# Performance work log

Hardware: AMD Instinct MI355X
Metric: run time of the kernel (lower is better)

## Reference

```python
import jax, jax.numpy as jnp
import numpy as np

B, C, H, W = 2048, 4, 84, 84
FEAT = 7 * 7 * 64  # 3136, from 84->20->9->7 conv arithmetic
D = 512
E = 6            # num_experts
K = 2            # top_k
A = 12           # output_dim (actions)


def _conv(x, w, b, stride):
    y = jax.lax.conv_general_dilated(
        x, w, window_strides=(stride, stride), padding='VALID',
        dimension_numbers=('NCHW', 'OIHW', 'NCHW'))
    return y + b[None, :, None, None]


def setup_inputs() -> dict:
    key = jax.random.key(0)
    ks = jax.random.split(key, 16)
    s = lambda k, shape, fan: jax.random.normal(k, shape, jnp.float32) * (1.0 / np.sqrt(fan))
    return {
        'x': jax.random.normal(ks[0], (B, C, H, W), jnp.float32),
        'c1_w': s(ks[1], (32, C, 8, 8), C * 64), 'c1_b': jnp.zeros((32,), jnp.float32),
        'c2_w': s(ks[2], (64, 32, 4, 4), 32 * 16), 'c2_b': jnp.zeros((64,), jnp.float32),
        'c3_w': s(ks[3], (64, 64, 3, 3), 64 * 9), 'c3_b': jnp.zeros((64,), jnp.float32),
        'fc_w': s(ks[4], (FEAT, D), FEAT), 'fc_b': jnp.zeros((D,), jnp.float32),
        'gate_w': s(ks[5], (D, E), D), 'gate_b': jnp.zeros((E,), jnp.float32),
        'e_w1': s(ks[6], (E, D, D), D), 'e_b1': jnp.zeros((E, D), jnp.float32),
        'e_w2': s(ks[7], (E, D, D), D), 'e_b2': jnp.zeros((E, D), jnp.float32),
        'e_w3': s(ks[8], (E, D, A), D), 'e_b3': jnp.zeros((E, A), jnp.float32),
    }


def reference(x, c1_w, c1_b, c2_w, c2_b, c3_w, c3_b, fc_w, fc_b,
              gate_w, gate_b, e_w1, e_b1, e_w2, e_b2, e_w3, e_b3):
    # CNN feature extractor (dropout omitted: eval semantics)
    h = jax.nn.relu(_conv(x, c1_w, c1_b, 4))
    h = jax.nn.relu(_conv(h, c2_w, c2_b, 2))
    h = jax.nn.relu(_conv(h, c3_w, c3_b, 1))
    h = h.reshape(h.shape[0], -1)                     # [B, 3136] (C,H,W flatten order)
    f = jax.nn.relu(h @ fc_w + fc_b)                  # [B, 512]

    # Gating: softmax -> top-2 -> renormalize
    gate_probs = jax.nn.softmax(f @ gate_w + gate_b, axis=-1)    # [B, E]
    top_p, top_i = jax.lax.top_k(gate_probs, K)                   # [B, K]
    top_p = top_p / jnp.sum(top_p, axis=-1, keepdims=True)

    # Experts: compute all (tiny MLPs), then gather top-k outputs
    h1 = jax.nn.relu(jnp.einsum('bd,edh->beh', f, e_w1) + e_b1)   # [B, E, D]
    h2 = jax.nn.relu(jnp.einsum('beh,ehg->beg', h1, e_w2) + e_b2) # [B, E, D]
    eo = jnp.einsum('beg,ego->beo', h2, e_w3) + e_b3              # [B, E, A]
    sel = jnp.take_along_axis(eo, top_i[:, :, None], axis=1)      # [B, K, A]
    out = jnp.sum(sel * top_p[:, :, None], axis=1)                # [B, A]
    return out
```

## Files before the change

kernel.cpp:

```cpp
#include <hip/hip_runtime.h>
#include <hip/hip_bf16.h>
#include <math.h>

typedef __attribute__((ext_vector_type(8))) short bf16x8;
typedef __attribute__((ext_vector_type(4))) float f32x4;

__device__ __forceinline__ float b2f(unsigned short u) {
    unsigned int v = ((unsigned int)u) << 16;
    return __uint_as_float(v);
}
__device__ __forceinline__ unsigned short f2b(float f) {
    __hip_bfloat16 h = __float2bfloat16(f);
    return *reinterpret_cast<unsigned short*>(&h);
}
__device__ __forceinline__ void split_trunc(float v, short& h, short& l) {
    unsigned int ui = __float_as_uint(v);
    h = (short)(ui >> 16);
    float hf = __uint_as_float(ui & 0xffff0000u);
    l = (short)f2b(v - hf);
}

__global__ __launch_bounds__(256) void prep_w(
    const float* __restrict__ w1, const float* __restrict__ w2, const float* __restrict__ w3,
    const float* __restrict__ ew3,
    unsigned short* __restrict__ wb1h, unsigned short* __restrict__ wb1l,
    unsigned short* __restrict__ w2h, unsigned short* __restrict__ w2l,
    unsigned short* __restrict__ w3h, unsigned short* __restrict__ w3l,
    float* __restrict__ w3t) {
    int tid = blockIdx.x * 256 + threadIdx.x;
    if (tid < 8192) {
        int k = tid >> 8, r = tid & 255;
        int c = r >> 6, ky = (r >> 3) & 7, kx = r & 7;
        float v = w1[tid];
        unsigned short h = f2b(v);
        int d = ((ky * 2 + (k >> 4)) * 16 + (k & 15)) * 32 + c * 8 + kx;
        wb1h[d] = h;
        wb1l[d] = f2b(v - b2f(h));
    } else if (tid < 8192 + 32768) {
        int i = tid - 8192;
        int n = i >> 9, r = i & 511;
        int c = r >> 4, ky = (r >> 2) & 3, kx = r & 3;
        float v = w2[i];
        unsigned short h = f2b(v);
        int d = ((ky * 4 + kx) * 64 + n) * 32 + c;
        w2h[d] = h;
        w2l[d] = f2b(v - b2f(h));
    } else if (tid < 8192 + 32768 + 36864) {
        int i = tid - 40960;
        int n = i / 576, r = i - n * 576;
        int c = r / 9, s = r - c * 9;
        int ky = s / 3, kx = s - ky * 3;
        float v = w3[i];
        unsigned short h = f2b(v);
        int d = (((ky * 3 + kx) * 2 + (c >> 5)) * 64 + n) * 32 + (c & 31);
        w3h[d] = h;
        w3l[d] = f2b(v - b2f(h));
    } else if (tid < 77824 + 36864) {
        int i = tid - 77824;
        int e = i / 6144, rem = i - e * 6144;
        int a = rem >> 9, k = rem & 511;
        w3t[i] = ew3[e * 6144 + k * 12 + a];
    }
}

__global__ __launch_bounds__(256) void prep_fcw(
    const float* __restrict__ fw, unsigned short* __restrict__ h, unsigned short* __restrict__ l) {
    __shared__ float tile[64][65];
    int k0 = blockIdx.x * 64;
    int n0 = blockIdx.y * 64;
    int tx = threadIdx.x & 63, ty = threadIdx.x >> 6;
#pragma unroll
    for (int j = 0; j < 16; j++) {
        int kk = ty + j * 4;
        int kp = k0 + kk;
        int p = kp >> 6, c = kp & 63;
        tile[kk][tx] = fw[(c * 49 + p) * 512 + n0 + tx];
    }
    __syncthreads();
#pragma unroll
    for (int j = 0; j < 16; j++) {
        int r = ty + j * 4;
        float v = tile[tx][r];
        unsigned short hh = f2b(v);
        long d = (long)(n0 + r) * 3136 + k0 + tx;
        h[d] = hh;
        l[d] = f2b(v - b2f(hh));
    }
}

__global__ __launch_bounds__(256) void prep_ewT(
    const float* __restrict__ ew1, const float* __restrict__ ew2,
    unsigned short* __restrict__ t1, unsigned short* __restrict__ t2) {
    __shared__ float tile[32][33];
    int z = blockIdx.z;
    int e = z % 6;
    const float* src = (z < 6) ? (ew1 + e * 262144) : (ew2 + e * 262144);
    unsigned short* dst = (z < 6) ? (t1 + e * 262144) : (t2 + e * 262144);
    int d0 = blockIdx.y * 32;
    int h0 = blockIdx.x * 32;
    int tx = threadIdx.x, ty = threadIdx.y;
#pragma unroll
    for (int j = 0; j < 4; j++)
        tile[ty + j * 8][tx] = src[(d0 + ty + j * 8) * 512 + h0 + tx];
    __syncthreads();
#pragma unroll
    for (int j = 0; j < 4; j++)
        dst[(h0 + ty + j * 8) * 512 + (d0 + tx)] = f2b(tile[tx][ty + j * 8]);
}

__global__ __launch_bounds__(256, 3) void conv1_k(
    const float* __restrict__ x, const unsigned short* __restrict__ wbh,
    const unsigned short* __restrict__ wbl, const float* __restrict__ b1,
    unsigned short* __restrict__ yhi, unsigned short* __restrict__ ylo) {
    int t = threadIdx.x;
    int wave = t >> 6, lane = t & 63, l16 = lane & 15, quad = lane >> 4;
    int px0 = blockIdx.x * 256 + wave * 64;
    const float* abase[4];
#pragma unroll
    for (int i = 0; i < 4; i++) {
        int px = px0 + i * 16 + l16;
        int n = px / 400;
        int rem = px - n * 400;
        int oy = rem / 20;
        int ox = rem - oy * 20;
        abase[i] = x + (long)n * 28224 + quad * 7056 + oy * 4 * 84 + ox * 4;
    }
    f32x4 acc[4][2];
#pragma unroll
    for (int i = 0; i < 4; i++)
#pragma unroll
        for (int j = 0; j < 2; j++)
#pragma unroll
            for (int r = 0; r < 4; r++) acc[i][j][r] = 0.f;
    float4 cur[8];
#pragma unroll
    for (int i = 0; i < 4; i++) {
        cur[i * 2] = *(const float4*)abase[i];
        cur[i * 2 + 1] = *(const float4*)(abase[i] + 4);
    }
#pragma unroll
    for (int ky = 0; ky < 8; ky++) {
        float4 nxt[8];
        if (ky < 7) {
#pragma unroll
            for (int i = 0; i < 4; i++) {
                const float* p = abase[i] + (ky + 1) * 84;
                nxt[i * 2] = *(const float4*)p;
                nxt[i * 2 + 1] = *(const float4*)(p + 4);
            }
        }
        int wo = (ky * 32 + l16) * 32 + quad * 8;
        bf16x8 bh0 = *(const bf16x8*)(wbh + wo);
        bf16x8 bh1 = *(const bf16x8*)(wbh + wo + 512);
        bf16x8 bl0 = *(const bf16x8*)(wbl + wo);
        bf16x8 bl1 = *(const bf16x8*)(wbl + wo + 512);
        bf16x8 ah[4], al[4];
#pragma unroll
        for (int i = 0; i < 4; i++) {
            float v[8] = {cur[i * 2].x, cur[i * 2].y, cur[i * 2].z, cur[i * 2].w,
                          cur[i * 2 + 1].x, cur[i * 2 + 1].y, cur[i * 2 + 1].z, cur[i * 2 + 1].w};
#pragma unroll
            for (int j = 0; j < 8; j++) {
                short hh, ll;
                split_trunc(v[j], hh, ll);
                ah[i][j] = hh;
                al[i][j] = ll;
            }
        }
#pragma unroll
        for (int i = 0; i < 4; i++) {
            acc[i][0] = __builtin_amdgcn_mfma_f32_16x16x32_bf16(ah[i], bh0, acc[i][0], 0, 0, 0);
            acc[i][0] = __builtin_amdgcn_mfma_f32_16x16x32_bf16(al[i], bh0, acc[i][0], 0, 0, 0);
            acc[i][0] = __builtin_amdgcn_mfma_f32_16x16x32_bf16(ah[i], bl0, acc[i][0], 0, 0, 0);
            acc[i][1] = __builtin_amdgcn_mfma_f32_16x16x32_bf16(ah[i], bh1, acc[i][1], 0, 0, 0);
            acc[i][1] = __builtin_amdgcn_mfma_f32_16x16x32_bf16(al[i], bh1, acc[i][1], 0, 0, 0);
            acc[i][1] = __builtin_amdgcn_mfma_f32_16x16x32_bf16(ah[i], bl1, acc[i][1], 0, 0, 0);
        }
        if (ky < 7) {
#pragma unroll
            for (int q = 0; q < 8; q++) cur[q] = nxt[q];
        }
    }
    float bias0 = b1[l16], bias1 = b1[16 + l16];
#pragma unroll
    for (int i = 0; i < 4; i++) {
#pragma unroll
        for (int r = 0; r < 4; r++) {
            long px = px0 + i * 16 + quad * 4 + r;
            long o = px * 32;
            float v0 = fmaxf(acc[i][0][r] + bias0, 0.f);
            float v1 = fmaxf(acc[i][1][r] + bias1, 0.f);
            short h0, l0, h1, l1;
            split_trunc(v0, h0, l0);
            split_trunc(v1, h1, l1);
            yhi[o + l16] = (unsigned short)h0;
            ylo[o + l16] = (unsigned short)l0;
            yhi[o + 16 + l16] = (unsigned short)h1;
            ylo[o + 16 + l16] = (unsigned short)l1;
        }
    }
}

template <int C, int IH, int IW, int OH, int OW, int S, int KH, int KW>
__global__ __launch_bounds__(64, 3) void convm_k(
    const unsigned short* __restrict__ xhi, const unsigned short* __restrict__ xlo,
    const unsigned short* __restrict__ whi, const unsigned short* __restrict__ wlo,
    const float* __restrict__ bias,
    unsigned short* __restrict__ yhi, unsigned short* __restrict__ ylo) {
    constexpr int CH = C / 32;
    constexpr int NCHUNK = KH * KW * CH;
    int lane = threadIdx.x, l16 = lane & 15, quad = lane >> 4;
    int pxbase = blockIdx.x * 64;
    long xoff[4];
#pragma unroll
    for (int i = 0; i < 4; i++) {
        int px = pxbase + i * 16 + l16;
        int n = px / (OH * OW);
        int rem = px - n * (OH * OW);
        int oy = rem / OW;
        int ox = rem - oy * OW;
        xoff[i] = (((long)n * IH + oy * S) * IW + ox * S) * C + quad * 8;
    }
    f32x4 acc[4][4];
#pragma unroll
    for (int i = 0; i < 4; i++)
#pragma unroll
        for (int j = 0; j < 4; j++)
#pragma unroll
            for (int r = 0; r < 4; r++) acc[i][j][r] = 0.f;
#pragma unroll 2
    for (int ck = 0; ck < NCHUNK; ck++) {
        int kyx = ck / CH;
        int ch = ck - kyx * CH;
        int ky = kyx / KW, kx = kyx - ky * KW;
        long koff = ((long)(ky * IW + kx)) * C + ch * 32;
        bf16x8 ah[4], al[4], bh[4], bl[4];
#pragma unroll
        for (int i = 0; i < 4; i++) {
            ah[i] = *(const bf16x8*)(xhi + xoff[i] + koff);
            al[i] = *(const bf16x8*)(xlo + xoff[i] + koff);
        }
#pragma unroll
        for (int j = 0; j < 4; j++) {
            long b = ((long)ck * 64 + j * 16 + l16) * 32 + quad * 8;
            bh[j] = *(const bf16x8*)(whi + b);
            bl[j] = *(const bf16x8*)(wlo + b);
        }
#pragma unroll
        for (int i = 0; i < 4; i++)
#pragma unroll
            for (int j = 0; j < 4; j++) {
                acc[i][j] = __builtin_amdgcn_mfma_f32_16x16x32_bf16(ah[i], bh[j], acc[i][j], 0, 0, 0);
                acc[i][j] = __builtin_amdgcn_mfma_f32_16x16x32_bf16(ah[i], bl[j], acc[i][j], 0, 0, 0);
                acc[i][j] = __builtin_amdgcn_mfma_f32_16x16x32_bf16(al[i], bh[j], acc[i][j], 0, 0, 0);
            }
    }
#pragma unroll
    for (int i = 0; i < 4; i++)
#pragma unroll
        for (int j = 0; j < 4; j++) {
            int col = j * 16 + l16;
            float bv = bias[col];
#pragma unroll
            for (int r = 0; r < 4; r++) {
                int prow = pxbase + i * 16 + quad * 4 + r;
                float v = fmaxf(acc[i][j][r] + bv, 0.f);
                unsigned short h = f2b(v);
                yhi[(long)prow * 64 + col] = h;
                ylo[(long)prow * 64 + col] = f2b(v - b2f(h));
            }
        }
}

__global__ __launch_bounds__(64, 3) void fc_k(
    const unsigned short* __restrict__ Ahi, const unsigned short* __restrict__ Alo,
    const unsigned short* __restrict__ Bhi, const unsigned short* __restrict__ Blo,
    float* __restrict__ Cp) {
    int lane = threadIdx.x, l16 = lane & 15, quad = lane >> 4;
    int m0 = blockIdx.x * 64, n0 = blockIdx.y * 64;
    int z = blockIdx.z;
    int kBase = z * 448;
    f32x4 acc[4][4];
#pragma unroll
    for (int i = 0; i < 4; i++)
#pragma unroll
        for (int j = 0; j < 4; j++)
#pragma unroll
            for (int r = 0; r < 4; r++) acc[i][j][r] = 0.f;
#pragma unroll 2
    for (int k0 = kBase; k0 < kBase + 448; k0 += 32) {
        bf16x8 ah[4], al[4], bh[4], bl[4];
#pragma unroll
        for (int i = 0; i < 4; i++) {
            long a = (long)(m0 + i * 16 + l16) * 3136 + k0 + quad * 8;
            ah[i] = *(const bf16x8*)(Ahi + a);
            al[i] = *(const bf16x8*)(Alo + a);
        }
#pragma unroll
        for (int j = 0; j < 4; j++) {
            long b = (long)(n0 + j * 16 + l16) * 3136 + k0 + quad * 8;
            bh[j] = *(const bf16x8*)(Bhi + b);
            bl[j] = *(const bf16x8*)(Blo + b);
        }
#pragma unroll
        for (int i = 0; i < 4; i++)
#pragma unroll
            for (int j = 0; j < 4; j++) {
                acc[i][j] = __builtin_amdgcn_mfma_f32_16x16x32_bf16(ah[i], bh[j], acc[i][j], 0, 0, 0);
                acc[i][j] = __builtin_amdgcn_mfma_f32_16x16x32_bf16(ah[i], bl[j], acc[i][j], 0, 0, 0);
                acc[i][j] = __builtin_amdgcn_mfma_f32_16x16x32_bf16(al[i], bh[j], acc[i][j], 0, 0, 0);
            }
    }
    float* Cz = Cp + (long)z * 1048576;
#pragma unroll
    for (int i = 0; i < 4; i++)
#pragma unroll
        for (int j = 0; j < 4; j++) {
            int col = n0 + j * 16 + l16;
#pragma unroll
            for (int r = 0; r < 4; r++) {
                int row = m0 + i * 16 + quad * 4 + r;
                Cz[row * 512 + col] = acc[i][j][r];
            }
        }
}

__global__ __launch_bounds__(256) void fc_fin(
    const float* __restrict__ Cp, const float* __restrict__ bias,
    float* __restrict__ f, unsigned short* __restrict__ fb) {
    int tid = blockIdx.x * 256 + threadIdx.x;
    int col = tid & 511;
    float v = bias[col];
#pragma unroll
    for (int z = 0; z < 7; z++) v += Cp[tid + (long)z * 1048576];
    v = fmaxf(v, 0.f);
    f[tid] = v;
    fb[tid] = f2b(v);
}

__global__ __launch_bounds__(256) void gate_k(
    const float* __restrict__ f, const float* __restrict__ gw, const float* __restrict__ gb,
    int* __restrict__ topi, float* __restrict__ topp) {
    int wave = threadIdx.x >> 6, lane = threadIdx.x & 63;
    int row = blockIdx.x * 4 + wave;
    float fv[8];
#pragma unroll
    for (int j = 0; j < 8; j++) fv[j] = f[row * 512 + lane + 64 * j];
    float lg[6];
#pragma unroll
    for (int e = 0; e < 6; e++) {
        float a = 0.f;
#pragma unroll
        for (int j = 0; j < 8; j++) a += fv[j] * gw[(lane + 64 * j) * 6 + e];
#pragma unroll
        for (int off = 32; off > 0; off >>= 1) a += __shfl_xor(a, off, 64);
        lg[e] = a + gb[e];
    }
    if (lane == 0) {
        int i1 = 0;
        float v1 = lg[0];
#pragma unroll
        for (int e = 1; e < 6; e++)
            if (lg[e] > v1) { v1 = lg[e]; i1 = e; }
        int i2 = (i1 == 0) ? 1 : 0;
        float v2 = lg[i2];
#pragma unroll
        for (int e = 0; e < 6; e++)
            if (e != i1 && lg[e] > v2) { v2 = lg[e]; i2 = e; }
        float pa = 1.f / (1.f + expf(v2 - v1));
        topi[row * 2] = i1;
        topi[row * 2 + 1] = i2;
        topp[row * 2] = pa;
        topp[row * 2 + 1] = 1.f - pa;
    }
}

__global__ __launch_bounds__(64, 4) void moe_gemm(
    const unsigned short* __restrict__ A, long aStride,
    const unsigned short* __restrict__ Bt, const float* __restrict__ bias,
    unsigned short* __restrict__ C) {
    int e = blockIdx.z;
    const unsigned short* Ae = A + (long)e * aStride;
    const unsigned short* Be = Bt + (long)e * 262144;
    const float* be = bias + e * 512;
    unsigned short* Ce = C + (long)e * 2048 * 512;
    int lane = threadIdx.x, l16 = lane & 15, quad = lane >> 4;
    int m0 = blockIdx.x * 64, n0 = blockIdx.y * 64;
    f32x4 acc[4][4];
#pragma unroll
    for (int i = 0; i < 4; i++)
#pragma unroll
        for (int j = 0; j < 4; j++)
#pragma unroll
            for (int r = 0; r < 4; r++) acc[i][j][r] = 0.f;
#pragma unroll 4
    for (int k0 = 0; k0 < 512; k0 += 32) {
        bf16x8 a[4], b[4];
#pragma unroll
        for (int i = 0; i < 4; i++)
            a[i] = *(const bf16x8*)(Ae + (long)(m0 + i * 16 + l16) * 512 + k0 + quad * 8);
#pragma unroll
        for (int j = 0; j < 4; j++)
            b[j] = *(const bf16x8*)(Be + (long)(n0 + j * 16 + l16) * 512 + k0 + quad * 8);
#pragma unroll
        for (int i = 0; i < 4; i++)
#pragma unroll
            for (int j = 0; j < 4; j++)
                acc[i][j] = __builtin_amdgcn_mfma_f32_16x16x32_bf16(a[i], b[j], acc[i][j], 0, 0, 0);
    }
#pragma unroll
    for (int i = 0; i < 4; i++)
#pragma unroll
        for (int j = 0; j < 4; j++) {
            int col = n0 + j * 16 + l16;
            float bcol = be[col];
#pragma unroll
            for (int r = 0; r < 4; r++) {
                int row = m0 + i * 16 + quad * 4 + r;
                float v = fmaxf(acc[i][j][r] + bcol, 0.f);
                Ce[(long)row * 512 + col] = f2b(v);
            }
        }
}

__global__ __launch_bounds__(256) void combine_k(
    const unsigned short* __restrict__ h2, const float* __restrict__ w3t,
    const float* __restrict__ b3, const int* __restrict__ topi,
    const float* __restrict__ topp, float* __restrict__ out) {
    int b = blockIdx.x * 4 + (threadIdx.x >> 6);
    int lane = threadIdx.x & 63;
    int e0 = topi[b * 2], e1 = topi[b * 2 + 1];
    float p0 = topp[b * 2], p1 = topp[b * 2 + 1];
    float r[12];
#pragma unroll
    for (int a = 0; a < 12; a++) r[a] = 0.f;
#pragma unroll
    for (int j = 0; j < 2; j++) {
        int e = j ? e1 : e0;
        float p = j ? p1 : p0;
        const unsigned short* hp = h2 + ((long)e * 2048 + b) * 512 + lane * 8;
        bf16x8 hv = *(const bf16x8*)hp;
        float hf[8];
#pragma unroll
        for (int q = 0; q < 8; q++) hf[q] = b2f((unsigned short)hv[q]);
        const float* wb = w3t + e * 6144 + lane * 8;
#pragma unroll
        for (int a = 0; a < 12; a++) {
            float4 w0 = *(const float4*)(wb + a * 512);
            float4 w1 = *(const float4*)(wb + a * 512 + 4);
            float acc = hf[0] * w0.x + hf[1] * w0.y + hf[2] * w0.z + hf[3] * w0.w +
                        hf[4] * w1.x + hf[5] * w1.y + hf[6] * w1.z + hf[7] * w1.w;
            r[a] += p * acc;
        }
    }
#pragma unroll
    for (int a = 0; a < 12; a++)
#pragma unroll
        for (int off = 32; off > 0; off >>= 1) r[a] += __shfl_xor(r[a], off, 64);
    float v = 0.f;
#pragma unroll
    for (int a = 0; a < 12; a++)
        if (lane == a) v = r[a];
    if (lane < 12)
        out[b * 12 + lane] = v + p0 * b3[e0 * 12 + lane] + p1 * b3[e1 * 12 + lane];
}

extern "C" void kernel_launch(void* const* d_in, const int* in_sizes, int n_in,
                              void* d_out, int out_size, void* d_ws, size_t ws_size,
                              hipStream_t stream) {
    const float* x   = (const float*)d_in[0];
    const float* c1w = (const float*)d_in[1];
    const float* c1b = (const float*)d_in[2];
    const float* c2w = (const float*)d_in[3];
    const float* c2b = (const float*)d_in[4];
    const float* c3w = (const float*)d_in[5];
    const float* c3b = (const float*)d_in[6];
    const float* fcw = (const float*)d_in[7];
    const float* fcb = (const float*)d_in[8];
    const float* gw  = (const float*)d_in[9];
    const float* gb  = (const float*)d_in[10];
    const float* ew1 = (const float*)d_in[11];
    const float* eb1 = (const float*)d_in[12];
    const float* ew2 = (const float*)d_in[13];
    const float* eb2 = (const float*)d_in[14];
    const float* ew3 = (const float*)d_in[15];
    const float* eb3 = (const float*)d_in[16];

    char* ws = (char*)d_ws;
    unsigned short* y1hi = (unsigned short*)(ws + 0L);
    unsigned short* y1lo = (unsigned short*)(ws + 52428800L);
    unsigned short* f3hi = (unsigned short*)(ws + 0L);
    unsigned short* f3lo = (unsigned short*)(ws + 12845056L);
    unsigned short* y2hi = (unsigned short*)(ws + 104857600L);
    unsigned short* y2lo = (unsigned short*)(ws + 126091264L);
    unsigned short* h1   = (unsigned short*)(ws + 104857600L);
    unsigned short* h2   = (unsigned short*)(ws + 117440512L);
    float* f             = (float*)(ws + 147324928L);
    unsigned short* fb   = (unsigned short*)(ws + 151519232L);
    int*   topi          = (int*)(ws + 153616384L);
    float* topp          = (float*)(ws + 153632768L);
    unsigned short* w2h  = (unsigned short*)(ws + 153681920L);
    unsigned short* w2l  = (unsigned short*)(ws + 153747456L);
    unsigned short* w3h  = (unsigned short*)(ws + 153812992L);
    unsigned short* w3l  = (unsigned short*)(ws + 153886720L);
    unsigned short* fcwh = (unsigned short*)(ws + 153960448L);
    unsigned short* fcwl = (unsigned short*)(ws + 157171712L);
    unsigned short* ew1t = (unsigned short*)(ws + 160382976L);
    unsigned short* ew2t = (unsigned short*)(ws + 163528704L);
    float* w3t           = (float*)(ws + 166674432L);
    float* Cp            = (float*)(ws + 166821888L);
    unsigned short* wb1h = (unsigned short*)(ws + 196182016L);
    unsigned short* wb1l = (unsigned short*)(ws + 196198400L);
    float* out = (float*)d_out;

    hipLaunchKernelGGL(prep_w, dim3(448), dim3(256), 0, stream, c1w, c2w, c3w, ew3,
                       wb1h, wb1l, w2h, w2l, w3h, w3l, w3t);
    hipLaunchKernelGGL(prep_fcw, dim3(49, 8), dim3(256), 0, stream, fcw, fcwh, fcwl);
    hipLaunchKernelGGL(prep_ewT, dim3(16, 16, 12), dim3(32, 8), 0, stream, ew1, ew2, ew1t, ew2t);
    hipLaunchKernelGGL(conv1_k, dim3(3200), dim3(256), 0, stream, x, wb1h, wb1l, c1b, y1hi, y1lo);
    hipLaunchKernelGGL((convm_k<32, 20, 20, 9, 9, 2, 4, 4>), dim3(2592), dim3(64), 0, stream,
                       y1hi, y1lo, w2h, w2l, c2b, y2hi, y2lo);
    hipLaunchKernelGGL((convm_k<64, 9, 9, 7, 7, 1, 3, 3>), dim3(1568), dim3(64), 0, stream,
                       y2hi, y2lo, w3h, w3l, c3b, f3hi, f3lo);
    hipLaunchKernelGGL(fc_k, dim3(32, 8, 7), dim3(64), 0, stream, f3hi, f3lo, fcwh, fcwl, Cp);
    hipLaunchKernelGGL(fc_fin, dim3(4096), dim3(256), 0, stream, Cp, fcb, f, fb);
    hipLaunchKernelGGL(gate_k, dim3(512), dim3(256), 0, stream, f, gw, gb, topi, topp);
    hipLaunchKernelGGL(moe_gemm, dim3(32, 8, 6), dim3(64), 0, stream, fb, 0L, ew1t, eb1, h1);
    hipLaunchKernelGGL(moe_gemm, dim3(32, 8, 6), dim3(64), 0, stream, h1, 1048576L, ew2t, eb2, h2);
    hipLaunchKernelGGL(combine_k, dim3(512), dim3(256), 0, stream, h2, w3t, eb3, topi, topp, out);
}
```

Before: 712.0 us.

## Route MoE experts sparsely, stage conv1 input in LDS, merge prep and gate kernels

```diff
diff --git a/kernel.cpp b/kernel.cpp
--- a/kernel.cpp
+++ b/kernel.cpp
@@ -20,110 +20,116 @@
     l = (short)f2b(v - hf);
 }
 
-__global__ __launch_bounds__(256) void prep_w(
+__global__ __launch_bounds__(256) void prep_all(
     const float* __restrict__ w1, const float* __restrict__ w2, const float* __restrict__ w3,
-    const float* __restrict__ ew3,
+    const float* __restrict__ ew3, const float* __restrict__ fw,
+    const float* __restrict__ ew1, const float* __restrict__ ew2,
     unsigned short* __restrict__ wb1h, unsigned short* __restrict__ wb1l,
     unsigned short* __restrict__ w2h, unsigned short* __restrict__ w2l,
     unsigned short* __restrict__ w3h, unsigned short* __restrict__ w3l,
-    float* __restrict__ w3t) {
-    int tid = blockIdx.x * 256 + threadIdx.x;
-    if (tid < 8192) {
-        int k = tid >> 8, r = tid & 255;
-        int c = r >> 6, ky = (r >> 3) & 7, kx = r & 7;
-        float v = w1[tid];
-        unsigned short h = f2b(v);
-        int d = ((ky * 2 + (k >> 4)) * 16 + (k & 15)) * 32 + c * 8 + kx;
-        wb1h[d] = h;
-        wb1l[d] = f2b(v - b2f(h));
-    } else if (tid < 8192 + 32768) {
-        int i = tid - 8192;
-        int n = i >> 9, r = i & 511;
-        int c = r >> 4, ky = (r >> 2) & 3, kx = r & 3;
-        float v = w2[i];
-        unsigned short h = f2b(v);
-        int d = ((ky * 4 + kx) * 64 + n) * 32 + c;
-        w2h[d] = h;
-        w2l[d] = f2b(v - b2f(h));
-    } else if (tid < 8192 + 32768 + 36864) {
-        int i = tid - 40960;
-        int n = i / 576, r = i - n * 576;
-        int c = r / 9, s = r - c * 9;
-        int ky = s / 3, kx = s - ky * 3;
-        float v = w3[i];
-        unsigned short h = f2b(v);
-        int d = (((ky * 3 + kx) * 2 + (c >> 5)) * 64 + n) * 32 + (c & 31);
-        w3h[d] = h;
-        w3l[d] = f2b(v - b2f(h));
-    } else if (tid < 77824 + 36864) {
-        int i = tid - 77824;
-        int e = i / 6144, rem = i - e * 6144;
-        int a = rem >> 9, k = rem & 511;
-        w3t[i] = ew3[e * 6144 + k * 12 + a];
-    }
-}
-
-__global__ __launch_bounds__(256) void prep_fcw(
-    const float* __restrict__ fw, unsigned short* __restrict__ h, unsigned short* __restrict__ l) {
-    __shared__ float tile[64][65];
-    int k0 = blockIdx.x * 64;
-    int n0 = blockIdx.y * 64;
-    int tx = threadIdx.x & 63, ty = threadIdx.x >> 6;
-#pragma unroll
-    for (int j = 0; j < 16; j++) {
-        int kk = ty + j * 4;
-        int kp = k0 + kk;
-        int p = kp >> 6, c = kp & 63;
-        tile[kk][tx] = fw[(c * 49 + p) * 512 + n0 + tx];
-    }
-    __syncthreads();
-#pragma unroll
-    for (int j = 0; j < 16; j++) {
-        int r = ty + j * 4;
-        float v = tile[tx][r];
-        unsigned short hh = f2b(v);
-        long d = (long)(n0 + r) * 3136 + k0 + tx;
-        h[d] = hh;
-        l[d] = f2b(v - b2f(hh));
-    }
-}
-
-__global__ __launch_bounds__(256) void prep_ewT(
-    const float* __restrict__ ew1, const float* __restrict__ ew2,
-    unsigned short* __restrict__ t1, unsigned short* __restrict__ t2) {
-    __shared__ float tile[32][33];
-    int z = blockIdx.z;
-    int e = z % 6;
-    const float* src = (z < 6) ? (ew1 + e * 262144) : (ew2 + e * 262144);
-    unsigned short* dst = (z < 6) ? (t1 + e * 262144) : (t2 + e * 262144);
-    int d0 = blockIdx.y * 32;
-    int h0 = blockIdx.x * 32;
-    int tx = threadIdx.x, ty = threadIdx.y;
-#pragma unroll
-    for (int j = 0; j < 4; j++)
-        tile[ty + j * 8][tx] = src[(d0 + ty + j * 8) * 512 + h0 + tx];
-    __syncthreads();
-#pragma unroll
-    for (int j = 0; j < 4; j++)
-        dst[(h0 + ty + j * 8) * 512 + (d0 + tx)] = f2b(tile[tx][ty + j * 8]);
-}
-
-__global__ __launch_bounds__(256, 3) void conv1_k(
+    float* __restrict__ w3t,
+    unsigned short* __restrict__ fcwh, unsigned short* __restrict__ fcwl,
+    unsigned short* __restrict__ ew1t, unsigned short* __restrict__ ew2t) {
+    __shared__ float tile[64 * 65];
+    int bid = blockIdx.x;
+    int t = threadIdx.x;
+    if (bid < 392) {
+        int k0 = (bid % 49) * 64, n0 = (bid / 49) * 64;
+        int tx = t & 63, ty = t >> 6;
+#pragma unroll
+        for (int j = 0; j < 16; j++) {
+            int kk = ty + j * 4;
+            int kp = k0 + kk;
+            int p = kp >> 6, c = kp & 63;
+            tile[kk * 65 + tx] = fw[(c * 49 + p) * 512 + n0 + tx];
+        }
+        __syncthreads();
+#pragma unroll
+        for (int j = 0; j < 16; j++) {
+            int r = ty + j * 4;
+            float v = tile[tx * 65 + r];
+            unsigned short hh = f2b(v);
+            long d = (long)(n0 + r) * 3136 + k0 + tx;
+            fcwh[d] = hh;
+            fcwl[d] = f2b(v - b2f(hh));
+        }
+    } else if (bid < 392 + 3072) {
+        int q = bid - 392;
+        int z = q >> 8, rem = q & 255;
+        int d0 = (rem >> 4) * 32;
+        int h0 = (rem & 15) * 32;
+        int e = z % 6;
+        const float* src = (z < 6) ? (ew1 + e * 262144) : (ew2 + e * 262144);
+        unsigned short* dst = (z < 6) ? (ew1t + e * 262144) : (ew2t + e * 262144);
+        int tx = t & 31, ty = t >> 5;
+#pragma unroll
+        for (int j = 0; j < 4; j++)
+            tile[(ty + j * 8) * 33 + tx] = src[(d0 + ty + j * 8) * 512 + h0 + tx];
+        __syncthreads();
+#pragma unroll
+        for (int j = 0; j < 4; j++)
+            dst[(h0 + ty + j * 8) * 512 + (d0 + tx)] = f2b(tile[tx * 33 + ty + j * 8]);
+    } else {
+        int tid = (bid - 3464) * 256 + t;
+        if (tid < 8192) {
+            int k = tid >> 8, r = tid & 255;
+            int c = r >> 6, ky = (r >> 3) & 7, kx = r & 7;
+            float v = w1[tid];
+            unsigned short h = f2b(v);
+            int d = ((ky * 2 + (k >> 4)) * 16 + (k & 15)) * 32 + c * 8 + kx;
+            wb1h[d] = h;
+            wb1l[d] = f2b(v - b2f(h));
+        } else if (tid < 8192 + 32768) {
+            int i = tid - 8192;
+            int n = i >> 9, r = i & 511;
+            int c = r >> 4, ky = (r >> 2) & 3, kx = r & 3;
+            float v = w2[i];
+            unsigned short h = f2b(v);
+            int d = ((ky * 4 + kx) * 64 + n) * 32 + c;
+            w2h[d] = h;
+            w2l[d] = f2b(v - b2f(h));
+        } else if (tid < 8192 + 32768 + 36864) {
+            int i = tid - 40960;
+            int n = i / 576, r = i - n * 576;
+            int c = r / 9, s = r - c * 9;
+            int ky = s / 3, kx = s - ky * 3;
+            float v = w3[i];
+            unsigned short h = f2b(v);
+            int d = (((ky * 3 + kx) * 2 + (c >> 5)) * 64 + n) * 32 + (c & 31);
+            w3h[d] = h;
+            w3l[d] = f2b(v - b2f(h));
+        } else if (tid < 77824 + 36864) {
+            int i = tid - 77824;
+            int e = i / 6144, rem = i - e * 6144;
+            int a = rem >> 9, k = rem & 511;
+            w3t[i] = ew3[e * 6144 + k * 12 + a];
+        }
+    }
+}
+
+__global__ __launch_bounds__(256, 2) void conv1_k(
     const float* __restrict__ x, const unsigned short* __restrict__ wbh,
     const unsigned short* __restrict__ wbl, const float* __restrict__ b1,
     unsigned short* __restrict__ yhi, unsigned short* __restrict__ ylo) {
+    __shared__ float xs[14784];
+    int n = blockIdx.x >> 1, h = blockIdx.x & 1;
     int t = threadIdx.x;
+#pragma unroll
+    for (int c = 0; c < 4; c++) {
+        const float4* src = (const float4*)x + (long)(n * 4 + c) * 1764 + h * 840;
+        float4* dst = (float4*)xs + c * 924;
+        for (int i = t; i < 924; i += 256) dst[i] = src[i];
+    }
+    __syncthreads();
     int wave = t >> 6, lane = t & 63, l16 = lane & 15, quad = lane >> 4;
-    int px0 = blockIdx.x * 256 + wave * 64;
-    const float* abase[4];
-#pragma unroll
-    for (int i = 0; i < 4; i++) {
-        int px = px0 + i * 16 + l16;
-        int n = px / 400;
-        int rem = px - n * 400;
-        int oy = rem / 20;
-        int ox = rem - oy * 20;
-        abase[i] = x + (long)n * 28224 + quad * 7056 + oy * 4 * 84 + ox * 4;
+    int pyr[4], oxr[4];
+#pragma unroll
+    for (int ti = 0; ti < 4; ti++) {
+        int tile = wave + ti * 4;
+        int p = tile * 16 + l16;
+        p = p > 199 ? 199 : p;
+        pyr[ti] = p / 20;
+        oxr[ti] = p - pyr[ti] * 20;
     }
     f32x4 acc[4][2];
 #pragma unroll
@@ -132,71 +138,57 @@
         for (int j = 0; j < 2; j++)
 #pragma unroll
             for (int r = 0; r < 4; r++) acc[i][j][r] = 0.f;
-    float4 cur[8];
-#pragma unroll
-    for (int i = 0; i < 4; i++) {
-        cur[i * 2] = *(const float4*)abase[i];
-        cur[i * 2 + 1] = *(const float4*)(abase[i] + 4);
-    }
-#pragma unroll
+#pragma unroll 2
     for (int ky = 0; ky < 8; ky++) {
-        float4 nxt[8];
-        if (ky < 7) {
-#pragma unroll
-            for (int i = 0; i < 4; i++) {
-                const float* p = abase[i] + (ky + 1) * 84;
-                nxt[i * 2] = *(const float4*)p;
-                nxt[i * 2 + 1] = *(const float4*)(p + 4);
-            }
-        }
         int wo = (ky * 32 + l16) * 32 + quad * 8;
         bf16x8 bh0 = *(const bf16x8*)(wbh + wo);
         bf16x8 bh1 = *(const bf16x8*)(wbh + wo + 512);
         bf16x8 bl0 = *(const bf16x8*)(wbl + wo);
         bf16x8 bl1 = *(const bf16x8*)(wbl + wo + 512);
-        bf16x8 ah[4], al[4];
-#pragma unroll
-        for (int i = 0; i < 4; i++) {
-            float v[8] = {cur[i * 2].x, cur[i * 2].y, cur[i * 2].z, cur[i * 2].w,
-                          cur[i * 2 + 1].x, cur[i * 2 + 1].y, cur[i * 2 + 1].z, cur[i * 2 + 1].w};
+#pragma unroll
+        for (int ti = 0; ti < 4; ti++) {
+            int tile = wave + ti * 4;
+            if (tile > 12) break;
+            int addr = quad * 3696 + (pyr[ti] * 4 + ky) * 84 + oxr[ti] * 4;
+            float4 a0 = *(const float4*)&xs[addr];
+            float4 a1 = *(const float4*)&xs[addr + 4];
+            float v[8] = {a0.x, a0.y, a0.z, a0.w, a1.x, a1.y, a1.z, a1.w};
+            bf16x8 ah, al;
 #pragma unroll
             for (int j = 0; j < 8; j++) {
                 short hh, ll;
                 split_trunc(v[j], hh, ll);
-                ah[i][j] = hh;
-                al[i][j] = ll;
-            }
-        }
-#pragma unroll
-        for (int i = 0; i < 4; i++) {
-            acc[i][0] = __builtin_amdgcn_mfma_f32_16x16x32_bf16(ah[i], bh0, acc[i][0], 0, 0, 0);
-            acc[i][0] = __builtin_amdgcn_mfma_f32_16x16x32_bf16(al[i], bh0, acc[i][0], 0, 0, 0);
-            acc[i][0] = __builtin_amdgcn_mfma_f32_16x16x32_bf16(ah[i], bl0, acc[i][0], 0, 0, 0);
-            acc[i][1] = __builtin_amdgcn_mfma_f32_16x16x32_bf16(ah[i], bh1, acc[i][1], 0, 0, 0);
-            acc[i][1] = __builtin_amdgcn_mfma_f32_16x16x32_bf16(al[i], bh1, acc[i][1], 0, 0, 0);
-            acc[i][1] = __builtin_amdgcn_mfma_f32_16x16x32_bf16(ah[i], bl1, acc[i][1], 0, 0, 0);
-        }
-        if (ky < 7) {
-#pragma unroll
-            for (int q = 0; q < 8; q++) cur[q] = nxt[q];
+                ah[j] = hh;
+                al[j] = ll;
+            }
+            acc[ti][0] = __builtin_amdgcn_mfma_f32_16x16x32_bf16(ah, bh0, acc[ti][0], 0, 0, 0);
+            acc[ti][0] = __builtin_amdgcn_mfma_f32_16x16x32_bf16(al, bh0, acc[ti][0], 0, 0, 0);
+            acc[ti][0] = __builtin_amdgcn_mfma_f32_16x16x32_bf16(ah, bl0, acc[ti][0], 0, 0, 0);
+            acc[ti][1] = __builtin_amdgcn_mfma_f32_16x16x32_bf16(ah, bh1, acc[ti][1], 0, 0, 0);
+            acc[ti][1] = __builtin_amdgcn_mfma_f32_16x16x32_bf16(al, bh1, acc[ti][1], 0, 0, 0);
+            acc[ti][1] = __builtin_amdgcn_mfma_f32_16x16x32_bf16(ah, bl1, acc[ti][1], 0, 0, 0);
         }
     }
     float bias0 = b1[l16], bias1 = b1[16 + l16];
 #pragma unroll
-    for (int i = 0; i < 4; i++) {
+    for (int ti = 0; ti < 4; ti++) {
+        int tile = wave + ti * 4;
+        if (tile > 12) break;
 #pragma unroll
         for (int r = 0; r < 4; r++) {
-            long px = px0 + i * 16 + quad * 4 + r;
-            long o = px * 32;
-            float v0 = fmaxf(acc[i][0][r] + bias0, 0.f);
-            float v1 = fmaxf(acc[i][1][r] + bias1, 0.f);
-            short h0, l0, h1, l1;
-            split_trunc(v0, h0, l0);
-            split_trunc(v1, h1, l1);
-            yhi[o + l16] = (unsigned short)h0;
-            ylo[o + l16] = (unsigned short)l0;
-            yhi[o + 16 + l16] = (unsigned short)h1;
-            ylo[o + 16 + l16] = (unsigned short)l1;
+            int p = tile * 16 + quad * 4 + r;
+            if (p < 200) {
+                long o = ((long)n * 400 + h * 200 + p) * 32;
+                float v0 = fmaxf(acc[ti][0][r] + bias0, 0.f);
+                float v1 = fmaxf(acc[ti][1][r] + bias1, 0.f);
+                short h0, l0, h1, l1;
+                split_trunc(v0, h0, l0);
+                split_trunc(v1, h1, l1);
+                yhi[o + l16] = (unsigned short)h0;
+                ylo[o + l16] = (unsigned short)l0;
+                yhi[o + 16 + l16] = (unsigned short)h1;
+                ylo[o + 16 + l16] = (unsigned short)l1;
+            }
         }
     }
 }
@@ -265,9 +257,9 @@
             for (int r = 0; r < 4; r++) {
                 int prow = pxbase + i * 16 + quad * 4 + r;
                 float v = fmaxf(acc[i][j][r] + bv, 0.f);
-                unsigned short h = f2b(v);
-                yhi[(long)prow * 64 + col] = h;
-                ylo[(long)prow * 64 + col] = f2b(v - b2f(h));
+                unsigned short hh = f2b(v);
+                yhi[(long)prow * 64 + col] = hh;
+                ylo[(long)prow * 64 + col] = f2b(v - b2f(hh));
             }
         }
 }
@@ -275,7 +267,9 @@
 __global__ __launch_bounds__(64, 3) void fc_k(
     const unsigned short* __restrict__ Ahi, const unsigned short* __restrict__ Alo,
     const unsigned short* __restrict__ Bhi, const unsigned short* __restrict__ Blo,
-    float* __restrict__ Cp) {
+    float* __restrict__ Cp, int* __restrict__ cnt) {
+    if (blockIdx.x == 0 && blockIdx.y == 0 && blockIdx.z == 0 && threadIdx.x < 8)
+        cnt[threadIdx.x] = 0;
     int lane = threadIdx.x, l16 = lane & 15, quad = lane >> 4;
     int m0 = blockIdx.x * 64, n0 = blockIdx.y * 64;
     int z = blockIdx.z;
@@ -325,27 +319,25 @@
         }
 }
 
-__global__ __launch_bounds__(256) void fc_fin(
+__global__ __launch_bounds__(256) void fin_gate(
     const float* __restrict__ Cp, const float* __restrict__ bias,
-    float* __restrict__ f, unsigned short* __restrict__ fb) {
-    int tid = blockIdx.x * 256 + threadIdx.x;
-    int col = tid & 511;
-    float v = bias[col];
-#pragma unroll
-    for (int z = 0; z < 7; z++) v += Cp[tid + (long)z * 1048576];
-    v = fmaxf(v, 0.f);
-    f[tid] = v;
-    fb[tid] = f2b(v);
-}
-
-__global__ __launch_bounds__(256) void gate_k(
-    const float* __restrict__ f, const float* __restrict__ gw, const float* __restrict__ gb,
-    int* __restrict__ topi, float* __restrict__ topp) {
+    const float* __restrict__ gw, const float* __restrict__ gb,
+    unsigned short* __restrict__ fb, int* __restrict__ topi, float* __restrict__ topp,
+    int* __restrict__ cnt, int* __restrict__ list, int* __restrict__ pos) {
     int wave = threadIdx.x >> 6, lane = threadIdx.x & 63;
     int row = blockIdx.x * 4 + wave;
     float fv[8];
 #pragma unroll
-    for (int j = 0; j < 8; j++) fv[j] = f[row * 512 + lane + 64 * j];
+    for (int j = 0; j < 8; j++) {
+        int col = lane + 64 * j;
+        long idx = (long)row * 512 + col;
+        float v = bias[col];
+#pragma unroll
+        for (int z = 0; z < 7; z++) v += Cp[idx + (long)z * 1048576];
+        v = fmaxf(v, 0.f);
+        fv[j] = v;
+        fb[idx] = f2b(v);
+    }
     float lg[6];
 #pragma unroll
     for (int e = 0; e < 6; e++) {
@@ -372,20 +364,38 @@
         topi[row * 2 + 1] = i2;
         topp[row * 2] = pa;
         topp[row * 2 + 1] = 1.f - pa;
+        int s0 = atomicAdd(&cnt[i1], 1);
+        list[i1 * 2048 + s0] = row;
+        pos[row * 2] = s0;
+        int s1 = atomicAdd(&cnt[i2], 1);
+        list[i2 * 2048 + s1] = row;
+        pos[row * 2 + 1] = s1;
     }
 }
 
 __global__ __launch_bounds__(64, 4) void moe_gemm(
-    const unsigned short* __restrict__ A, long aStride,
+    const unsigned short* __restrict__ A, long aStride, int gather,
     const unsigned short* __restrict__ Bt, const float* __restrict__ bias,
+    const int* __restrict__ cnt, const int* __restrict__ list,
     unsigned short* __restrict__ C) {
     int e = blockIdx.z;
+    int M = cnt[e];
+    int m0 = blockIdx.x * 64;
+    if (m0 >= M) return;
     const unsigned short* Ae = A + (long)e * aStride;
     const unsigned short* Be = Bt + (long)e * 262144;
     const float* be = bias + e * 512;
-    unsigned short* Ce = C + (long)e * 2048 * 512;
+    unsigned short* Ce = C + (long)e * 1048576;
     int lane = threadIdx.x, l16 = lane & 15, quad = lane >> 4;
-    int m0 = blockIdx.x * 64, n0 = blockIdx.y * 64;
+    int n0 = blockIdx.y * 64;
+    long abase[4];
+#pragma unroll
+    for (int i = 0; i < 4; i++) {
+        int idx = m0 + i * 16 + l16;
+        idx = idx < M ? idx : M - 1;
+        int row = gather ? list[e * 2048 + idx] : idx;
+        abase[i] = (long)row * 512;
+    }
     f32x4 acc[4][4];
 #pragma unroll
     for (int i = 0; i < 4; i++)
@@ -398,7 +408,7 @@
         bf16x8 a[4], b[4];
 #pragma unroll
         for (int i = 0; i < 4; i++)
-            a[i] = *(const bf16x8*)(Ae + (long)(m0 + i * 16 + l16) * 512 + k0 + quad * 8);
+            a[i] = *(const bf16x8*)(Ae + abase[i] + k0 + quad * 8);
 #pragma unroll
         for (int j = 0; j < 4; j++)
             b[j] = *(const bf16x8*)(Be + (long)(n0 + j * 16 + l16) * 512 + k0 + quad * 8);
@@ -416,9 +426,11 @@
             float bcol = be[col];
 #pragma unroll
             for (int r = 0; r < 4; r++) {
-                int row = m0 + i * 16 + quad * 4 + r;
-                float v = fmaxf(acc[i][j][r] + bcol, 0.f);
-                Ce[(long)row * 512 + col] = f2b(v);
+                int idx = m0 + i * 16 + quad * 4 + r;
+                if (idx < M) {
+                    float v = fmaxf(acc[i][j][r] + bcol, 0.f);
+                    Ce[(long)idx * 512 + col] = f2b(v);
+                }
             }
         }
 }
@@ -426,7 +438,8 @@
 __global__ __launch_bounds__(256) void combine_k(
     const unsigned short* __restrict__ h2, const float* __restrict__ w3t,
     const float* __restrict__ b3, const int* __restrict__ topi,
-    const float* __restrict__ topp, float* __restrict__ out) {
+    const int* __restrict__ pos, const float* __restrict__ topp,
+    float* __restrict__ out) {
     int b = blockIdx.x * 4 + (threadIdx.x >> 6);
     int lane = threadIdx.x & 63;
     int e0 = topi[b * 2], e1 = topi[b * 2 + 1];
@@ -438,7 +451,8 @@
     for (int j = 0; j < 2; j++) {
         int e = j ? e1 : e0;
         float p = j ? p1 : p0;
-        const unsigned short* hp = h2 + ((long)e * 2048 + b) * 512 + lane * 8;
+        int s = pos[b * 2 + j];
+        const unsigned short* hp = h2 + ((long)e * 2048 + s) * 512 + lane * 8;
         bf16x8 hv = *(const bf16x8*)hp;
         float hf[8];
 #pragma unroll
@@ -495,7 +509,6 @@
     unsigned short* y2lo = (unsigned short*)(ws + 126091264L);
     unsigned short* h1   = (unsigned short*)(ws + 104857600L);
     unsigned short* h2   = (unsigned short*)(ws + 117440512L);
-    float* f             = (float*)(ws + 147324928L);
     unsigned short* fb   = (unsigned short*)(ws + 151519232L);
     int*   topi          = (int*)(ws + 153616384L);
     float* topp          = (float*)(ws + 153632768L);
@@ -511,21 +524,26 @@
     float* Cp            = (float*)(ws + 166821888L);
     unsigned short* wb1h = (unsigned short*)(ws + 196182016L);
     unsigned short* wb1l = (unsigned short*)(ws + 196198400L);
+    int* list            = (int*)(ws + 196214784L);
+    int* pos             = (int*)(ws + 196263936L);
+    int* cnt             = (int*)(ws + 196280320L);
     float* out = (float*)d_out;
 
-    hipLaunchKernelGGL(prep_w, dim3(448), dim3(256), 0, stream, c1w, c2w, c3w, ew3,
-                       wb1h, wb1l, w2h, w2l, w3h, w3l, w3t);
-    hipLaunchKernelGGL(prep_fcw, dim3(49, 8), dim3(256), 0, stream, fcw, fcwh, fcwl);
-    hipLaunchKernelGGL(prep_ewT, dim3(16, 16, 12), dim3(32, 8), 0, stream, ew1, ew2, ew1t, ew2t);
-    hipLaunchKernelGGL(conv1_k, dim3(3200), dim3(256), 0, stream, x, wb1h, wb1l, c1b, y1hi, y1lo);
+    hipLaunchKernelGGL(prep_all, dim3(3912), dim3(256), 0, stream,
+                       c1w, c2w, c3w, ew3, fcw, ew1, ew2,
+                       wb1h, wb1l, w2h, w2l, w3h, w3l, w3t, fcwh, fcwl, ew1t, ew2t);
+    hipLaunchKernelGGL(conv1_k, dim3(4096), dim3(256), 0, stream, x, wb1h, wb1l, c1b, y1hi, y1lo);
     hipLaunchKernelGGL((convm_k<32, 20, 20, 9, 9, 2, 4, 4>), dim3(2592), dim3(64), 0, stream,
                        y1hi, y1lo, w2h, w2l, c2b, y2hi, y2lo);
     hipLaunchKernelGGL((convm_k<64, 9, 9, 7, 7, 1, 3, 3>), dim3(1568), dim3(64), 0, stream,
                        y2hi, y2lo, w3h, w3l, c3b, f3hi, f3lo);
-    hipLaunchKernelGGL(fc_k, dim3(32, 8, 7), dim3(64), 0, stream, f3hi, f3lo, fcwh, fcwl, Cp);
-    hipLaunchKernelGGL(fc_fin, dim3(4096), dim3(256), 0, stream, Cp, fcb, f, fb);
-    hipLaunchKernelGGL(gate_k, dim3(512), dim3(256), 0, stream, f, gw, gb, topi, topp);
-    hipLaunchKernelGGL(moe_gemm, dim3(32, 8, 6), dim3(64), 0, stream, fb, 0L, ew1t, eb1, h1);
-    hipLaunchKernelGGL(moe_gemm, dim3(32, 8, 6), dim3(64), 0, stream, h1, 1048576L, ew2t, eb2, h2);
-    hipLaunchKernelGGL(combine_k, dim3(512), dim3(256), 0, stream, h2, w3t, eb3, topi, topp, out);
-}
+    hipLaunchKernelGGL(fc_k, dim3(32, 8, 7), dim3(64), 0, stream, f3hi, f3lo, fcwh, fcwl, Cp, cnt);
+    hipLaunchKernelGGL(fin_gate, dim3(512), dim3(256), 0, stream, Cp, fcb, gw, gb,
+                       fb, topi, topp, cnt, list, pos);
+    hipLaunchKernelGGL(moe_gemm, dim3(32, 8, 6), dim3(64), 0, stream,
+                       fb, 0L, 1, ew1t, eb1, cnt, list, h1);
+    hipLaunchKernelGGL(moe_gemm, dim3(32, 8, 6), dim3(64), 0, stream,
+                       h1, 1048576L, 0, ew2t, eb2, cnt, list, h2);
+    hipLaunchKernelGGL(combine_k, dim3(512), dim3(256), 0, stream,
+                       h2, w3t, eb3, topi, pos, topp, out);
+}
```

Result: slower. 796.5 us (+11.9%).
